# Optimization experiments

Hardware: AMD Instinct MI355X
Metric: run time of the kernel (lower is better)

The kernel has to match this reference:

```python
import jax, jax.numpy as jnp
import numpy as np

EPS = 1e-6
AREA_WIDTH = 3
NHEAD = 8
DIM = 16


def _skew(v):
    # v: [N,3] -> [N,3,3] cross-product matrix
    x, y, z = v[..., 0], v[..., 1], v[..., 2]
    zero = jnp.zeros_like(x)
    return jnp.stack([
        jnp.stack([zero, -z, y], -1),
        jnp.stack([z, zero, -x], -1),
        jnp.stack([-y, x, zero], -1)], -2)


def _create_meshgrid(h, w):
    # kornia create_meshgrid(..., normalized=False): last dim is (x, y), row-major flatten
    xs = jnp.arange(w, dtype=jnp.float32)
    ys = jnp.arange(h, dtype=jnp.float32)
    gx, gy = jnp.meshgrid(xs, ys, indexing='xy')  # [h,w]
    return jnp.stack([gx, gy], -1).reshape(h * w, 2)  # [S,2]


def _epipolar_lines(coord, R, t, K0, K1):
    # coord [S,2]; R [N,3,3]; t [N,3,1] -> lines [N,S,3] (unit-normalized a,b), mode [N,S]
    S = coord.shape[0]
    p = jnp.concatenate([coord, jnp.ones((S, 1), coord.dtype)], -1)  # [S,3]
    E = _skew(t[..., 0]) @ R                                         # [t]_x R
    F = jnp.swapaxes(jnp.linalg.inv(K1), -1, -2) @ E @ jnp.linalg.inv(K0)
    lines = jnp.einsum('nij,sj->nsi', F, p)
    n = jnp.linalg.norm(lines[..., :2], axis=-1, keepdims=True)
    lines = lines / jnp.maximum(n, 1e-12)
    mode = jnp.abs(lines[..., 1]) >= jnp.abs(lines[..., 0])  # True: solve y(x) (|b|>=|a|)
    return lines, mode


def _get_mask(lines, mode, coord, area_width):
    # lines [N,L,3], mode [N,L], coord [S,2] -> within [N,L,S]
    a, b, c = lines[..., 0], lines[..., 1], lines[..., 2]
    xs, ys = coord[:, 0], coord[:, 1]
    hw = area_width / 2.0
    safe = lambda d: jnp.where(jnp.abs(d) < 1e-12, 1e-12, d)
    cy = (-a / safe(b))[..., None] * xs + (-c / safe(b))[..., None]  # [N,L,S]
    cx = (-b / safe(a))[..., None] * ys + (-c / safe(a))[..., None]
    wy = (ys < cy + hw) & (ys > cy - hw)
    wx = (xs < cx + hw) & (xs > cx - hw)
    return jnp.where(mode[..., None], wy, wx)


def _gather_index(within, C):
    # sort-based top-C compaction, index 0 doubles as padding (faithful to source)
    S = within.shape[-1]
    idx = jnp.arange(S, dtype=jnp.int32)
    ti = jnp.where(within, idx[None, None, :], 0)
    ti = jnp.sort(ti, axis=-1)[..., -C:]
    return ti, ti != 0


def _feature_map(x):
    return jax.nn.elu(x) + 1.0


def reference(queries, keys, values, solved_sample, K0, K1, R, t, h0c, w0c, scale):
    N, L, H, D = queries.shape
    sol = np.asarray(solved_sample).astype(bool)  # static split of the batch
    sol_idx = np.nonzero(sol)[0]
    uns_idx = np.nonzero(~sol)[0]
    Q = _feature_map(queries)
    K = _feature_map(keys)
    out = jnp.zeros((N, L, H, D), queries.dtype)

    if sol_idx.size > 0:  # epipolar-gathered candidate attention, direction '0to1'
        coord = _create_meshgrid(h0c, w0c)
        K0s = K0[sol_idx].at[:, :2, :].mul(1.0 / scale)
        K1s = K1[sol_idx].at[:, :2, :].mul(1.0 / scale)
        C = max(h0c, w0c) * AREA_WIDTH
        lines, mode = _epipolar_lines(coord, R[sol_idx], t[sol_idx], K0s, K1s)
        within = _get_mask(lines, mode, coord, AREA_WIDTH)       # [Ns,L,S]
        index, mask = _gather_index(within, C)                    # [Ns,L,C]
        Ns = sol_idx.size
        n_ix = jnp.arange(Ns)[:, None, None]
        Qs = Q[sol_idx]
        Ks = K[sol_idx][n_ix, index]            # [Ns,L,C,H,D]
        Vs = values[sol_idx][n_ix, index]
        m = mask[..., None, None].astype(Ks.dtype)
        Ks = Ks * m
        Vs = Vs * m / C
        KV = jnp.einsum('nlchd,nlchv->nlhdv', Ks, Vs)
        Z = 1.0 / (jnp.einsum('nlhd,nlhd->nlh', Qs, Ks.sum(2)) + EPS)
        out = out.at[sol_idx].set(jnp.einsum('nlhd,nlhdv,nlh->nlhv', Qs, KV, Z) * C)

    if uns_idx.size > 0:  # plain linear attention
        Qu, Ku, Vu = Q[uns_idx], K[uns_idx], values[uns_idx]
        S = Ku.shape[1]
        KV = jnp.einsum('nshd,nshv->nhdv', Ku, Vu / S)
        Z = 1.0 / (jnp.einsum('nlhd,nhd->nlh', Qu, Ku.sum(1)) + EPS)
        out = out.at[uns_idx].set(jnp.einsum('nlhd,nhdv,nlh->nlhv', Qu, KV, Z) * S)
    return out


def setup_inputs() -> dict:
    key = jax.random.key(0)
    kq, kk, kv = jax.random.split(key, 3)
    N, H, D = 4, NHEAD, DIM
    h0c, w0c = 48, 64
    L = h0c * w0c
    queries = jax.random.normal(kq, (N, L, H, D), jnp.float32)
    keys = jax.random.normal(kk, (N, L, H, D), jnp.float32)
    values = jax.random.normal(kv, (N, L, H, D), jnp.float32)
    solved_sample = jnp.array([True, True, False, False])
    Kmat = np.array([[600., 0., 256.], [0., 600., 192.], [0., 0., 1.]], np.float32)
    K0 = jnp.asarray(np.tile(Kmat, (N, 1, 1)))
    Rl, tl = [], []
    for i in range(N):
        th = 0.05 * (i + 1)
        Rl.append(np.array([[np.cos(th), 0., np.sin(th)], [0., 1., 0.],
                            [-np.sin(th), 0., np.cos(th)]], np.float32))
        tl.append(np.array([[0.2 + 0.01 * i], [0.05], [0.02]], np.float32))
    R = jnp.asarray(np.stack(Rl))
    t = jnp.asarray(np.stack(tl))
    return {"queries": queries, "keys": keys, "values": values,
            "solved_sample": solved_sample, "K0": K0, "K1": K0, "R": R, "t": t,
            "h0c": h0c, "w0c": w0c, "scale": 8}
```

## Files before the change

kernel.cpp:

```cpp
#include <hip/hip_runtime.h>
#include <math.h>

#define NHEAD 8
#define DIM   16
#define EPSF  1e-6f
#define KVCH  8

typedef _Float16 half2_t __attribute__((ext_vector_type(2)));
typedef _Float16 half4_t __attribute__((ext_vector_type(4)));

#if defined(__has_builtin)
#if __has_builtin(__builtin_amdgcn_fdot2)
#define HAVE_FDOT2 1
#endif
#endif

__device__ __forceinline__ float dot2(half2_t a, half2_t b, float c) {
#ifdef HAVE_FDOT2
    return __builtin_amdgcn_fdot2(a, b, c, false);
#else
    return c + (float)a.x * (float)b.x + (float)a.y * (float)b.y;
#endif
}

__device__ __forceinline__ float4 f4add(float4 a, float4 b) {
    return make_float4(a.x + b.x, a.y + b.y, a.z + b.z, a.w + b.w);
}

__device__ __forceinline__ bool solved_flag(const void* p, int i) {
    const unsigned int* u = (const unsigned int*)p;
    unsigned int v0 = u[0];
    if (v0 <= 1u)             return u[i] != 0u;
    if (v0 == 0x3F800000u)    return ((const float*)p)[i] != 0.0f;
    return ((const unsigned char*)p)[i] != 0;
}

__device__ __forceinline__ float fm(float x) {
    return x > 0.f ? x + 1.f : expf(x);
}

__device__ void inv3d(const double* M, double* inv) {
    double det = M[0]*(M[4]*M[8]-M[5]*M[7]) - M[1]*(M[3]*M[8]-M[5]*M[6]) + M[2]*(M[3]*M[7]-M[4]*M[6]);
    double id = 1.0 / det;
    inv[0] =  (M[4]*M[8]-M[5]*M[7])*id;
    inv[1] = -(M[1]*M[8]-M[2]*M[7])*id;
    inv[2] =  (M[1]*M[5]-M[2]*M[4])*id;
    inv[3] = -(M[3]*M[8]-M[5]*M[6])*id;
    inv[4] =  (M[0]*M[8]-M[2]*M[6])*id;
    inv[5] = -(M[0]*M[5]-M[2]*M[3])*id;
    inv[6] =  (M[3]*M[7]-M[4]*M[6])*id;
    inv[7] = -(M[0]*M[7]-M[1]*M[6])*id;
    inv[8] =  (M[0]*M[4]-M[1]*M[3])*id;
}

__device__ void compute_F_one(const float* K0, const float* K1, const float* R,
                              const float* t, float invs, float* Fout, int n) {
    double A[9], B[9];
    for (int i = 0; i < 9; ++i) {
        float a = K0[n*9 + i], b = K1[n*9 + i];
        if (i < 6) { a *= invs; b *= invs; }
        A[i] = (double)a; B[i] = (double)b;
    }
    double iA[9], iB[9];
    inv3d(A, iA); inv3d(B, iB);
    double tx = t[n*3+0], ty = t[n*3+1], tz = t[n*3+2];
    double S[9] = {0.0,-tz,ty, tz,0.0,-tx, -ty,tx,0.0};
    double E[9], M[9];
    for (int i = 0; i < 3; ++i)
        for (int j = 0; j < 3; ++j) {
            double s = 0.0;
            for (int k = 0; k < 3; ++k) s += S[i*3+k] * (double)R[n*9 + k*3 + j];
            E[i*3+j] = s;
        }
    for (int i = 0; i < 3; ++i)
        for (int j = 0; j < 3; ++j) {
            double s = 0.0;
            for (int k = 0; k < 3; ++k) s += E[i*3+k] * iA[k*3+j];
            M[i*3+j] = s;
        }
    for (int i = 0; i < 3; ++i)
        for (int j = 0; j < 3; ++j) {
            double s = 0.0;
            for (int k = 0; k < 3; ++k) s += iB[k*3+i] * M[k*3+j];
            Fout[n*9 + i*3 + j] = (float)s;
        }
}

__launch_bounds__(256)
__global__ void prep_kv(const float4* __restrict__ Kr4, const float4* __restrict__ Vr4,
                        _Float16* __restrict__ KVh, int n4,
                        const float* __restrict__ Kr, const float* __restrict__ Vr,
                        const void* __restrict__ flags,
                        float* __restrict__ KVp, float* __restrict__ Ksp,
                        const float* __restrict__ K0, const float* __restrict__ K1,
                        const float* __restrict__ R,  const float* __restrict__ t,
                        const int* __restrict__ scale_p, float* __restrict__ Fout,
                        int N, int L, int PB) {
    __shared__ float kvred[4][256];
    __shared__ float ksred[4][16];
    if ((int)blockIdx.x < PB) {
        int i = blockIdx.x * 256 + threadIdx.x;
        if (i < n4) {
            float4 k = Kr4[i];
            float4 v = Vr4[i];
            half4_t kh = { (_Float16)fm(k.x), (_Float16)fm(k.y), (_Float16)fm(k.z), (_Float16)fm(k.w) };
            half4_t vh = { (_Float16)v.x, (_Float16)v.y, (_Float16)v.z, (_Float16)v.w };
            int r = i >> 5;
            int w = (i & 31) << 2;
            *(half4_t*)(KVh + (size_t)r * 256 + w)       = kh;
            *(half4_t*)(KVh + (size_t)r * 256 + 128 + w) = vh;
        }
        if (blockIdx.x == 0 && threadIdx.x < (unsigned)N) {
            float invs = 1.0f / (float)(*scale_p);
            compute_F_one(K0, K1, R, t, invs, Fout, threadIdx.x);
        }
    } else {
        int kb = blockIdx.x - PB;
        int chunk = kb & (KVCH - 1);
        int h = (kb >> 3) & 7;
        int n = kb >> 6;
        if (n >= N || solved_flag(flags, n)) return;

        int wv   = threadIdx.x >> 6;
        int lane = threadIdx.x & 63;

        int rowsPer = (L + KVCH - 1) / KVCH;
        int r0 = chunk * rowsPer;
        int r1 = min(r0 + rowsPer, L);
        int rowsW = ((rowsPer + 7) / 8) * 2;
        int w0 = r0 + wv * rowsW;
        int ngroups = rowsW >> 1;

        bool isV = lane >= 32;
        int srow_off = (lane >> 4) & 1;
        int elem = lane & 15;
        const float* bp = (isV ? Vr : Kr) + ((size_t)n * L) * (NHEAD * DIM) + h * DIM + elem;

        int d   = lane >> 2;
        int vv4 = (lane & 3) << 2;

        float acc0 = 0.f, acc1 = 0.f, acc2 = 0.f, acc3 = 0.f, ks = 0.f;

        #pragma unroll 4
        for (int g2 = 0; g2 < ngroups; ++g2) {
            int s = w0 + (g2 << 1) + srow_off;
            bool valid = s < r1;
            int sc = valid ? s : r0;
            float val = bp[(size_t)sc * (NHEAD * DIM)];
            if (!isV) val = fm(val);
            val = valid ? val : 0.f;
            float k0 = __shfl(val, d);
            float k1 = __shfl(val, 16 + d);
            float va0 = __shfl(val, 32 + vv4);
            float va1 = __shfl(val, 33 + vv4);
            float va2 = __shfl(val, 34 + vv4);
            float va3 = __shfl(val, 35 + vv4);
            float vb0 = __shfl(val, 48 + vv4);
            float vb1 = __shfl(val, 49 + vv4);
            float vb2 = __shfl(val, 50 + vv4);
            float vb3 = __shfl(val, 51 + vv4);
            acc0 = fmaf(k0, va0, acc0); acc0 = fmaf(k1, vb0, acc0);
            acc1 = fmaf(k0, va1, acc1); acc1 = fmaf(k1, vb1, acc1);
            acc2 = fmaf(k0, va2, acc2); acc2 = fmaf(k1, vb2, acc2);
            acc3 = fmaf(k0, va3, acc3); acc3 = fmaf(k1, vb3, acc3);
            ks += k0 + k1;
        }

        *(float4*)&kvred[wv][lane << 2] = make_float4(acc0, acc1, acc2, acc3);
        if ((lane & 3) == 0) ksred[wv][d] = ks;
        __syncthreads();
        if (wv == 0) {
            float4 rsum = f4add(f4add(*(float4*)&kvred[0][lane << 2],
                                      *(float4*)&kvred[1][lane << 2]),
                                f4add(*(float4*)&kvred[2][lane << 2],
                                      *(float4*)&kvred[3][lane << 2]));
            *(float4*)(KVp + (((size_t)chunk * N + n) * NHEAD + h) * 256 + (lane << 2)) = rsum;
            if (lane < 16)
                Ksp[(((size_t)chunk * N + n) * NHEAD + h) * 16 + lane] =
                    ksred[0][lane] + ksred[1][lane] + ksred[2][lane] + ksred[3][lane];
        }
    }
}

struct Buf {
    uint4 kl, kh, vl, vh;
    float msk;
};
union H16 { uint4 u; half2_t h[4]; _Float16 e[8]; };

__device__ __forceinline__ void issue(Buf& b, const char* KVb, int base16,
                                      float slope, float inter, int oo, float c1,
                                      int ob, int outerN, int innerMax, int sI, int sO) {
    int io = ob + oo;
    float fo = (float)io;
    float cc = fmaf(slope, fo, inter);
    float lo = cc - 1.5f;
    float fl = floorf(lo);
    float fi = fl + c1;
    int ii = (int)fi;
    bool val = (io < outerN) & (ii >= 0) & (ii < innerMax) & (fi > lo) & (fi < cc + 1.5f);
    int s2 = ii * sI + io * sO;
    val = val && (s2 != 0);
    int off = ((val ? s2 : 0) << 9) + base16;
    const char* p = KVb + off;
    b.kl = *(const uint4*)(p);
    b.kh = *(const uint4*)(p + 128);
    b.vl = *(const uint4*)(p + 256);
    b.vh = *(const uint4*)(p + 384);
    b.msk = val ? 1.f : 0.f;
}

__device__ __forceinline__ void consume(const Buf& b, const half2_t* ql, const half2_t* qh,
                                        float* aL, float* aH, float& dL, float& dH) {
    H16 k0, k1, v0, v1;
    k0.u = b.kl; k1.u = b.kh; v0.u = b.vl; v1.u = b.vh;
    float sA = 0.f, sB = 0.f;
    #pragma unroll
    for (int i = 0; i < 4; ++i) {
        sA = dot2(ql[i], k0.h[i], sA);
        sB = dot2(qh[i], k1.h[i], sB);
    }
    sA += __shfl_xor(sA, 1);
    sB += __shfl_xor(sB, 1);
    float scL = sA * b.msk;
    float scH = sB * b.msk;
    dL += scL; dH += scH;
    #pragma unroll
    for (int i = 0; i < 8; ++i) {
        aL[i] = fmaf(scL, (float)v0.e[i], aL[i]);
        aH[i] = fmaf(scH, (float)v1.e[i], aH[i]);
    }
}

__launch_bounds__(256)
__global__ void mega(const float* __restrict__ Qr,
                     const _Float16* __restrict__ KVh,
                     const void* __restrict__ flags,  const float* __restrict__ F,
                     const float* __restrict__ KVp,   const float* __restrict__ Ksp,
                     float* __restrict__ outp,
                     const int* __restrict__ h0c_p, const int* __restrict__ w0c_p,
                     int N, int L, int Bs) {
    if ((int)blockIdx.x < Bs) {
        int g  = blockIdx.x & 7;
        int gb = blockIdx.x >> 3;

        int scnt = 0, smap[8];
        for (int i = 0; i < N && i < 8; ++i)
            if (solved_flag(flags, i)) smap[scnt++] = i;
        if (scnt == 0) return;

        int r   = (g * scnt) >> 3;
        int g0  = (r * 8 + scnt - 1) / scnt;
        int ng  = ((r + 1) * 8 + scnt - 1) / scnt - g0;
        int sub = g - g0;
        int n   = smap[r];

        int wv  = threadIdx.x >> 6;
        int lane = threadIdx.x & 63;
        int q = (gb * ng + sub) * 4 + wv;
        if (q >= L) return;
        q = __builtin_amdgcn_readfirstlane(q);
        int qidx = n * L + q;

        int W  = *w0c_p;
        int Hc = *h0c_p;
        float px = (float)(q % W);
        float py = (float)(q / W);

        const float* Fn = F + n * 9;
        float a = Fn[0]*px + Fn[1]*py + Fn[2];
        float b = Fn[3]*px + Fn[4]*py + Fn[5];
        float c = Fn[6]*px + Fn[7]*py + Fn[8];
        float nrm = sqrtf(a*a + b*b);
        float mdiv = fmaxf(nrm, 1e-12f);
        a /= mdiv; b /= mdiv; c /= mdiv;
        bool mode = fabsf(b) >= fabsf(a);

        float slope, inter;
        int outerN, innerMax, sI, sO;
        if (mode) {
            float bs = (fabsf(b) < 1e-12f) ? 1e-12f : b;
            slope = -a / bs; inter = -c / bs;
            outerN = W; innerMax = Hc; sI = W; sO = 1;
        } else {
            float as = (fabsf(a) < 1e-12f) ? 1e-12f : a;
            slope = -b / as; inter = -c / as;
            outerN = Hc; innerMax = W; sI = 1; sO = W;
        }

        int cL   = lane >> 3;
        int sub8 = lane & 7;
        int hL   = sub8 >> 1;
        int dh   = sub8 & 1;
        int base16 = sub8 << 4;

        const float* qbase = Qr + (size_t)qidx * (NHEAD * DIM);
        half2_t ql[4], qh[4];
        {
            const float4* qa = (const float4*)(qbase + hL * DIM + dh * 8);
            float4 a0 = qa[0], a1 = qa[1];
            ql[0] = (half2_t){ (_Float16)fm(a0.x), (_Float16)fm(a0.y) };
            ql[1] = (half2_t){ (_Float16)fm(a0.z), (_Float16)fm(a0.w) };
            ql[2] = (half2_t){ (_Float16)fm(a1.x), (_Float16)fm(a1.y) };
            ql[3] = (half2_t){ (_Float16)fm(a1.z), (_Float16)fm(a1.w) };
            const float4* qb = (const float4*)(qbase + (hL + 4) * DIM + dh * 8);
            float4 b0 = qb[0], b1 = qb[1];
            qh[0] = (half2_t){ (_Float16)fm(b0.x), (_Float16)fm(b0.y) };
            qh[1] = (half2_t){ (_Float16)fm(b0.z), (_Float16)fm(b0.w) };
            qh[2] = (half2_t){ (_Float16)fm(b1.x), (_Float16)fm(b1.y) };
            qh[3] = (half2_t){ (_Float16)fm(b1.z), (_Float16)fm(b1.w) };
        }

        const char* KVb = (const char*)KVh + (size_t)n * L * 512;

        int mm0 = cL, mm1 = 8 + cL, mm2 = 16 + cL;
        int oo0 = mm0 / 3, oo1 = mm1 / 3, oo2 = mm2 / 3;
        float c10 = (float)(1 + (mm0 - 3 * oo0));
        float c11 = (float)(1 + (mm1 - 3 * oo1));
        float c12 = (float)(1 + (mm2 - 3 * oo2));

        int totalC = outerN * 3;
        int NM3 = (totalC + 23) / 24;

        float accL[8], accH[8];
        #pragma unroll
        for (int i = 0; i < 8; ++i) { accL[i] = 0.f; accH[i] = 0.f; }
        float denL = 0.f, denH = 0.f;

        for (int k = 0; k < NM3; ++k) {
            int ob = k << 3;
            Buf A, B, C;
            issue(A, KVb, base16, slope, inter, oo0, c10, ob, outerN, innerMax, sI, sO);
            issue(B, KVb, base16, slope, inter, oo1, c11, ob, outerN, innerMax, sI, sO);
            issue(C, KVb, base16, slope, inter, oo2, c12, ob, outerN, innerMax, sI, sO);
            consume(A, ql, qh, accL, accH, denL, denH);
            consume(B, ql, qh, accL, accH, denL, denH);
            consume(C, ql, qh, accL, accH, denL, denH);
        }

        #pragma unroll
        for (int j = 0; j < 8; ++j) {
            accL[j] += __shfl_xor(accL[j], 8);
            accL[j] += __shfl_xor(accL[j], 16);
            accL[j] += __shfl_xor(accL[j], 32);
            accH[j] += __shfl_xor(accH[j], 8);
            accH[j] += __shfl_xor(accH[j], 16);
            accH[j] += __shfl_xor(accH[j], 32);
        }
        denL += __shfl_xor(denL, 8);
        denL += __shfl_xor(denL, 16);
        denL += __shfl_xor(denL, 32);
        denH += __shfl_xor(denH, 8);
        denH += __shfl_xor(denH, 16);
        denH += __shfl_xor(denH, 32);

        if (lane < 8) {
            float rL = 1.0f / (denL + EPSF);
            float rH = 1.0f / (denH + EPSF);
            float* op = outp + (size_t)qidx * (NHEAD * DIM) + lane * 8;
            float4 o0 = { accL[0]*rL, accL[1]*rL, accL[2]*rL, accL[3]*rL };
            float4 o1 = { accL[4]*rL, accL[5]*rL, accL[6]*rL, accL[7]*rL };
            ((float4*)op)[0] = o0;
            ((float4*)op)[1] = o1;
            float4 o2 = { accH[0]*rH, accH[1]*rH, accH[2]*rH, accH[3]*rH };
            float4 o3 = { accH[4]*rH, accH[5]*rH, accH[6]*rH, accH[7]*rH };
            ((float4*)(op + 64))[0] = o2;
            ((float4*)(op + 64))[1] = o3;
        }
    } else {
        __shared__ float kvf[8 * 264];
        __shared__ float ksf[8 * 17];
        int t  = threadIdx.x;
        int ib = ((int)blockIdx.x - Bs) << 8;
        int ns0 = ib >> 6;
        int n   = ns0 / L;
        int nlast = (ns0 + 3) / L;
        if (n == nlast) {
            if (solved_flag(flags, n)) return;
            const float* KVpn = KVp + (size_t)n * (NHEAD * 256);
            float4 a0 = make_float4(0.f,0.f,0.f,0.f), a1 = make_float4(0.f,0.f,0.f,0.f);
            #pragma unroll
            for (int ch = 0; ch < KVCH; ++ch) {
                const float4* src = (const float4*)(KVpn + (size_t)ch * (N * NHEAD * 256));
                a0 = f4add(a0, src[2*t]);
                a1 = f4add(a1, src[2*t + 1]);
            }
            {
                int e = t << 3, hh = e >> 8, rr = e & 255;
                *(float4*)&kvf[hh * 264 + rr]     = a0;
                *(float4*)&kvf[hh * 264 + rr + 4] = a1;
            }
            if (t < 32) {
                const float* Kspn = Ksp + (size_t)n * (NHEAD * 16);
                float4 s4 = make_float4(0.f,0.f,0.f,0.f);
                #pragma unroll
                for (int ch = 0; ch < KVCH; ++ch)
                    s4 = f4add(s4, *(const float4*)(Kspn + (size_t)ch * (N * NHEAD * 16) + 4*t));
                int e2 = t << 2, h2 = e2 >> 4, d2 = e2 & 15;
                ksf[h2*17 + d2]     = s4.x;
                ksf[h2*17 + d2 + 1] = s4.y;
                ksf[h2*17 + d2 + 2] = s4.z;
                ksf[h2*17 + d2 + 3] = s4.w;
            }
            __syncthreads();
            int p = t & 63, h = p >> 3, v = (p & 7) * 2;
            int ns = ns0 + (t >> 6);
            const float4* q4 = (const float4*)(Qr + (size_t)ns * (NHEAD * DIM) + h * DIM);
            float4 Q0 = q4[0], Q1 = q4[1], Q2 = q4[2], Q3 = q4[3];
            float qd[16] = { fm(Q0.x), fm(Q0.y), fm(Q0.z), fm(Q0.w),
                             fm(Q1.x), fm(Q1.y), fm(Q1.z), fm(Q1.w),
                             fm(Q2.x), fm(Q2.y), fm(Q2.z), fm(Q2.w),
                             fm(Q3.x), fm(Q3.y), fm(Q3.z), fm(Q3.w) };
            const float* kvh_ = &kvf[h * 264 + v];
            const float* ksh_ = &ksf[h * 17];
            float num0 = 0.f, num1 = 0.f, den = 0.f;
            #pragma unroll
            for (int d = 0; d < 16; ++d) {
                float2 kv2 = *(const float2*)(kvh_ + (d << 4));
                num0 += qd[d] * kv2.x;
                num1 += qd[d] * kv2.y;
                den  += qd[d] * ksh_[d];
            }
            float rdiv = 1.0f / (den + EPSF);
            float2 o2 = { num0 * rdiv, num1 * rdiv };
            *(float2*)(outp + (size_t)ns * (NHEAD * DIM) + h * DIM + v) = o2;
        } else {
            long long tot2 = (long long)N * L * NHEAD * DIM / 2;
            long long idx2 = (long long)ib + t;
            if (idx2 >= tot2) return;
            int p = (int)(idx2 & 63);
            int h = p >> 3;
            int v = (p & 7) * 2;
            long long ns = idx2 >> 6;
            int nn = (int)(ns / L);
            if (solved_flag(flags, nn)) return;
            const float* qrow = Qr + ns * (NHEAD * DIM) + h * DIM;
            float num0 = 0.f, num1 = 0.f, den = 0.f;
            #pragma unroll
            for (int d = 0; d < 16; ++d) {
                float qdv = fm(qrow[d]);
                #pragma unroll
                for (int cch = 0; cch < KVCH; ++cch) {
                    const float2 kv2 = *(const float2*)(KVp + (((size_t)cch * N + nn) * NHEAD + h) * 256 + (d << 4) + v);
                    num0 += qdv * kv2.x;
                    num1 += qdv * kv2.y;
                    den  += qdv * Ksp[(((size_t)cch * N + nn) * NHEAD + h) * 16 + d];
                }
            }
            float rdiv = 1.0f / (den + EPSF);
            size_t ob = ns * (NHEAD * DIM) + h * DIM + v;
            outp[ob]     = num0 * rdiv;
            outp[ob + 1] = num1 * rdiv;
        }
    }
}

extern "C" void kernel_launch(void* const* d_in, const int* in_sizes, int n_in,
                              void* d_out, int out_size, void* d_ws, size_t ws_size,
                              hipStream_t stream) {
    const float* Qr   = (const float*)d_in[0];
    const float* Kr   = (const float*)d_in[1];
    const float* Vr   = (const float*)d_in[2];
    const void*  flag = d_in[3];
    const float* K0   = (const float*)d_in[4];
    const float* K1   = (const float*)d_in[5];
    const float* R    = (const float*)d_in[6];
    const float* t    = (const float*)d_in[7];
    const int*   h0c  = (const int*)d_in[8];
    const int*   w0c  = (const int*)d_in[9];
    const int*   scl  = (const int*)d_in[10];

    int N = in_sizes[3];
    int T = in_sizes[0];
    int L = T / (N * NHEAD * DIM);

    _Float16* KVh = (_Float16*)d_ws;
    float* Fm   = (float*)(KVh + (size_t)2 * T);
    float* KVp  = Fm + (size_t)N * 9;
    float* Ksp  = KVp + (size_t)KVCH * N * NHEAD * 256;

    float* outp = (float*)d_out;

    int n4 = T / 4;
    int PB = (n4 + 255) / 256;
    int KB = N * NHEAD * KVCH;
    prep_kv<<<PB + KB, 256, 0, stream>>>((const float4*)Kr, (const float4*)Vr,
                                         KVh, n4, Kr, Vr, flag, KVp, Ksp,
                                         K0, K1, R, t, scl, Fm, N, L, PB);

    int GB = (L + 7) / 8;
    int Bs = 8 * GB;
    long long tot2 = (long long)N * L * NHEAD * DIM / 2;
    int Bu = (int)((tot2 + 255) / 256);
    mega<<<Bs + Bu, 256, 0, stream>>>(Qr, KVh, flag, Fm, KVp, Ksp, outp,
                                      h0c, w0c, N, L, Bs);
}
```

Measured before the change: 143.1 us.

## Double-buffer KV gathers through LDS with async global_load_lds prefetch

Replaces the three-wide register-buffered gather loop with a software pipeline that streams each KV group directly into per-wave LDS buffers via global_load_lds, keeping two groups in flight while consuming the previous one. The goal is to hide gather latency and cut the register pressure of holding three buffers. The shared memory is unified into one 32KB array reused by the other branch. Manual vmcnt/lgkmcnt waits are fragile. The buffer rotation writes the new prefetch into the buffer just read, and the register fallback ignores the wait semantics.

```diff
diff --git a/kernel.cpp b/kernel.cpp
--- a/kernel.cpp
+++ b/kernel.cpp
@@ -13,7 +13,13 @@
 #if __has_builtin(__builtin_amdgcn_fdot2)
 #define HAVE_FDOT2 1
 #endif
+#if __has_builtin(__builtin_amdgcn_global_load_lds)
+#define HAVE_GLL 1
 #endif
+#endif
+
+#define GLOBAL_AS __attribute__((address_space(1)))
+#define LDS_AS    __attribute__((address_space(3)))
 
 __device__ __forceinline__ float dot2(half2_t a, half2_t b, float c) {
 #ifdef HAVE_FDOT2
@@ -182,38 +188,43 @@
     }
 }
 
-struct Buf {
-    uint4 kl, kh, vl, vh;
-    float msk;
-};
 union H16 { uint4 u; half2_t h[4]; _Float16 e[8]; };
 
-__device__ __forceinline__ void issue(Buf& b, const char* KVb, int base16,
-                                      float slope, float inter, int oo, float c1,
-                                      int ob, int outerN, int innerMax, int sI, int sO) {
+__device__ __forceinline__ float prefetch_grp(const char* KVb, char* ldsbuf, int base16,
+                                              float slope, float inter, int oo, float c1,
+                                              int ob, int outerN, int innerMax, int sI, int sO) {
     int io = ob + oo;
     float fo = (float)io;
     float cc = fmaf(slope, fo, inter);
     float lo = cc - 1.5f;
-    float fl = floorf(lo);
-    float fi = fl + c1;
+    float fi = floorf(lo) + c1;
     int ii = (int)fi;
     bool val = (io < outerN) & (ii >= 0) & (ii < innerMax) & (fi > lo) & (fi < cc + 1.5f);
     int s2 = ii * sI + io * sO;
     val = val && (s2 != 0);
     int off = ((val ? s2 : 0) << 9) + base16;
     const char* p = KVb + off;
-    b.kl = *(const uint4*)(p);
-    b.kh = *(const uint4*)(p + 128);
-    b.vl = *(const uint4*)(p + 256);
-    b.vh = *(const uint4*)(p + 384);
-    b.msk = val ? 1.f : 0.f;
-}
-
-__device__ __forceinline__ void consume(const Buf& b, const half2_t* ql, const half2_t* qh,
-                                        float* aL, float* aH, float& dL, float& dH) {
+#ifdef HAVE_GLL
+    #pragma unroll
+    for (int j = 0; j < 4; ++j)
+        __builtin_amdgcn_global_load_lds(
+            (const GLOBAL_AS unsigned int*)(p + (j << 7)),
+            (LDS_AS unsigned int*)(ldsbuf + (j << 10)),
+            16, 0, 0);
+#else
+    int lane = threadIdx.x & 63;
+    #pragma unroll
+    for (int j = 0; j < 4; ++j)
+        ((uint4*)(ldsbuf + (j << 10)))[lane] = *(const uint4*)(p + (j << 7));
+#endif
+    return val ? 1.f : 0.f;
+}
+
+__device__ __forceinline__ void consume4(uint4 ukl, uint4 ukh, uint4 uvl, uint4 uvh, float msk,
+                                         const half2_t* ql, const half2_t* qh,
+                                         float* aL, float* aH, float& dL, float& dH) {
     H16 k0, k1, v0, v1;
-    k0.u = b.kl; k1.u = b.kh; v0.u = b.vl; v1.u = b.vh;
+    k0.u = ukl; k1.u = ukh; v0.u = uvl; v1.u = uvh;
     float sA = 0.f, sB = 0.f;
     #pragma unroll
     for (int i = 0; i < 4; ++i) {
@@ -222,8 +233,8 @@
     }
     sA += __shfl_xor(sA, 1);
     sB += __shfl_xor(sB, 1);
-    float scL = sA * b.msk;
-    float scH = sB * b.msk;
+    float scL = sA * msk;
+    float scH = sB * msk;
     dL += scL; dH += scH;
     #pragma unroll
     for (int i = 0; i < 8; ++i) {
@@ -240,6 +251,7 @@
                      float* __restrict__ outp,
                      const int* __restrict__ h0c_p, const int* __restrict__ w0c_p,
                      int N, int L, int Bs) {
+    __shared__ __align__(16) char smem[32768];
     if ((int)blockIdx.x < Bs) {
         int g  = blockIdx.x & 7;
         int gb = blockIdx.x >> 3;
@@ -327,16 +339,33 @@
         for (int i = 0; i < 8; ++i) { accL[i] = 0.f; accH[i] = 0.f; }
         float denL = 0.f, denH = 0.f;
 
+        char* wbuf = smem + (wv << 13);
+        char* curB = wbuf;
+        char* nxtB = wbuf + 4096;
+        float mq0 = prefetch_grp(KVb, curB, base16, slope, inter, oo0, c10, 0, outerN, innerMax, sI, sO);
+        float mq1 = prefetch_grp(KVb, nxtB, base16, slope, inter, oo1, c11, 0, outerN, innerMax, sI, sO);
+
+        #define PHASE(OO, C1, OB)                                                              \
+        {                                                                                      \
+            asm volatile("s_waitcnt vmcnt(4)" ::: "memory");       \
+            const uint4* b4 = (const uint4*)curB;                                              \
+            uint4 kl = b4[lane], kh2 = b4[64 + lane], vl = b4[128 + lane], vh2 = b4[192 + lane];\
+            asm volatile("s_waitcnt lgkmcnt(0)" ::: "memory");    \
+            float nm = prefetch_grp(KVb, curB, base16, slope, inter, OO, C1, OB,               \
+                                    outerN, innerMax, sI, sO);                                 \
+            consume4(kl, kh2, vl, vh2, mq0, ql, qh, accL, accH, denL, denH);                   \
+            mq0 = mq1; mq1 = nm;                                                               \
+            char* tB = curB; curB = nxtB; nxtB = tB;                                           \
+        }
+
         for (int k = 0; k < NM3; ++k) {
-            int ob = k << 3;
-            Buf A, B, C;
-            issue(A, KVb, base16, slope, inter, oo0, c10, ob, outerN, innerMax, sI, sO);
-            issue(B, KVb, base16, slope, inter, oo1, c11, ob, outerN, innerMax, sI, sO);
-            issue(C, KVb, base16, slope, inter, oo2, c12, ob, outerN, innerMax, sI, sO);
-            consume(A, ql, qh, accL, accH, denL, denH);
-            consume(B, ql, qh, accL, accH, denL, denH);
-            consume(C, ql, qh, accL, accH, denL, denH);
-        }
+            int ob  = k << 3;
+            int obn = ob + 8;
+            PHASE(oo2, c12, ob);
+            PHASE(oo0, c10, obn);
+            PHASE(oo1, c11, obn);
+        }
+        #undef PHASE
 
         #pragma unroll
         for (int j = 0; j < 8; ++j) {
@@ -368,8 +397,8 @@
             ((float4*)(op + 64))[1] = o3;
         }
     } else {
-        __shared__ float kvf[8 * 264];
-        __shared__ float ksf[8 * 17];
+        float* kvf = (float*)smem;
+        float* ksf = (float*)(smem + 8448);
         int t  = threadIdx.x;
         int ib = ((int)blockIdx.x - Bs) << 8;
         int ns0 = ib >> 6;
```

Measured after the change: 148.5 us. 3.8% more time.
